# Kernel optimization log

Measured on AMD Instinct MI355X. Metric: run time of the kernel, lower is better.

## Reference

```python
import jax, jax.numpy as jnp
import numpy as np

N_NODES = 100000
N_EDGES = 1600000
D_IN, D_HID, N_CLASS = 256, 64, 40


def setup_inputs() -> dict:
    key = jax.random.key(0)
    ks = jax.random.split(key, 8)
    x = jax.random.normal(ks[0], (N_NODES, D_IN), dtype=jnp.float32)
    edge_src = jax.random.randint(ks[1], (N_EDGES,), 0, N_NODES, dtype=jnp.int64)
    edge_dst = jax.random.randint(ks[2], (N_EDGES,), 0, N_NODES, dtype=jnp.int64)
    edge_weight = jax.random.uniform(ks[3], (N_EDGES,), dtype=jnp.float32)
    W1 = jax.random.normal(ks[4], (D_IN, D_HID), dtype=jnp.float32) * (1.0 / np.sqrt(D_IN))
    b1 = jnp.zeros((D_HID,), dtype=jnp.float32)
    W2 = jax.random.normal(ks[5], (D_HID, N_CLASS), dtype=jnp.float32) * (1.0 / np.sqrt(D_HID))
    b2 = jnp.zeros((N_CLASS,), dtype=jnp.float32)
    return {"x": x, "edge_src": edge_src, "edge_dst": edge_dst,
            "edge_weight": edge_weight, "W1": W1, "b1": b1, "W2": W2, "b2": b2}


def _gcn_layer(h, W, b, edge_src, edge_dst, edge_weight):
    # support = h @ W  (dense transform), then sparse adj matmul:
    # out[dst] += w * support[src]
    support = h @ W                              # [N, d_out]
    msgs = edge_weight[:, None] * support[edge_src]  # [E, d_out] gather
    agg = jax.ops.segment_sum(msgs, edge_dst, num_segments=N_NODES)
    return agg + b


def reference(x, edge_src, edge_dst, edge_weight, W1, b1, W2, b2):
    # dropout prob = 0.0 -> identity (deterministic reference)
    h = _gcn_layer(x, W1, b1, edge_src, edge_dst, edge_weight)
    h = _gcn_layer(h, W2, b2, edge_src, edge_dst, edge_weight)
    return jax.nn.log_softmax(h, axis=1)
```

## Files before the change

kernel.cpp:

```cpp
#include <hip/hip_runtime.h>
#include <hip/hip_fp16.h>
#include <math.h>

#define N_NODES 100000
#define N_EDGES 1600000
#define D_IN    256
#define D_HID   64
#define N_CLASS 40

#define SCAN_CHUNK 256
#define SCAN_NB    ((N_NODES + SCAN_CHUNK - 1) / SCAN_CHUNK)
#define SLOT_MAX   48
#define GEMM_NB    ((N_NODES + 255) / 256)
#define FILL_NB    ((N_EDGES + 255) / 256)
#define TSTRIDE    64

__global__ __launch_bounds__(256) void prep_kernel(
    const float* __restrict__ W1, const float* __restrict__ W2,
    const float* __restrict__ b1, float* __restrict__ W12t, float* __restrict__ c1)
{
    int idx = blockIdx.x * 256 + threadIdx.x;
    if (idx < D_IN * N_CLASS) {
        int k = idx / N_CLASS;
        int c = idx - k * N_CLASS;
        float s = 0.f;
#pragma unroll
        for (int j = 0; j < D_HID; ++j)
            s = fmaf(W1[k * D_HID + j], W2[j * N_CLASS + c], s);
        W12t[c * D_IN + k] = s;
    }
    if (blockIdx.x == 0 && threadIdx.x < N_CLASS) {
        int c = threadIdx.x;
        float s = 0.f;
#pragma unroll
        for (int j = 0; j < D_HID; ++j)
            s = fmaf(b1[j], W2[j * N_CLASS + c], s);
        c1[c] = s;
    }
}

__device__ __forceinline__ void gemm_body(
    int gblk, int tid,
    const float* __restrict__ x, const float* __restrict__ W12t,
    __half* __restrict__ T, float* xs, float* wt)
{
    const int row0 = gblk * 256;

    for (int i = tid; i < N_CLASS * D_IN; i += 256) {
        int c = i >> 8;
        int k = i & 255;
        wt[c * 260 + k] = W12t[i];
    }

    const int rg = tid >> 2;
    const int cg = tid & 3;
    const int c0 = cg * 10;

    float acc[4][10];
#pragma unroll
    for (int r = 0; r < 4; ++r)
#pragma unroll
        for (int j = 0; j < 10; ++j) acc[r][j] = 0.f;

    const float4* x4 = (const float4*)x;
    float4* xs4 = (float4*)xs;
    const float4* wt4 = (const float4*)wt;

    for (int kb = 0; kb < 8; ++kb) {
        __syncthreads();
#pragma unroll
        for (int ph = 0; ph < 8; ++ph) {
            int i = ph * 256 + tid;
            int r  = i >> 3;
            int c4 = i & 7;
            int grow = min(row0 + r, N_NODES - 1);
            float4 v = x4[(size_t)grow * 64 + kb * 8 + c4];
            xs4[r * 8 + (c4 ^ ((r >> 2) & 7))] = v;
        }
        __syncthreads();

#pragma unroll
        for (int k4 = 0; k4 < 8; ++k4) {
            float4 xv[4];
#pragma unroll
            for (int r = 0; r < 4; ++r)
                xv[r] = xs4[(rg * 4 + r) * 8 + (k4 ^ (rg & 7))];
#pragma unroll
            for (int j = 0; j < 10; ++j) {
                float4 w = wt4[(c0 + j) * 65 + kb * 8 + k4];
#pragma unroll
                for (int r = 0; r < 4; ++r)
                    acc[r][j] = fmaf(xv[r].x, w.x,
                                fmaf(xv[r].y, w.y,
                                fmaf(xv[r].z, w.z,
                                fmaf(xv[r].w, w.w, acc[r][j]))));
            }
        }
    }

#pragma unroll
    for (int r = 0; r < 4; ++r) {
        int row = row0 + rg * 4 + r;
        if (row < N_NODES) {
            __half2* Trow = (__half2*)(T + (size_t)row * TSTRIDE + c0);
#pragma unroll
            for (int q = 0; q < 5; ++q)
                Trow[q] = __floats2half2_rn(acc[r][2 * q], acc[r][2 * q + 1]);
        }
    }
}

__global__ __launch_bounds__(256) void gemm_fill_kernel(
    const float* __restrict__ x, const float* __restrict__ W12t,
    __half* __restrict__ T,
    const int* __restrict__ esrc, const int* __restrict__ edst,
    const float* __restrict__ ew, int* __restrict__ cnt,
    int2* __restrict__ slots)
{
    __shared__ float xs[256 * 32];
    __shared__ float wt[N_CLASS * 260];
    const int tid = threadIdx.x;

    if (blockIdx.x < GEMM_NB) {
        gemm_body(blockIdx.x, tid, x, W12t, T, xs, wt);
    } else {
        int e = (blockIdx.x - GEMM_NB) * 256 + tid;
        if (e < N_EDGES) {
            int   d = edst[e];
            int   s = esrc[e];
            float w = ew[e];
            int slot = atomicAdd(&cnt[d], 1);
            if (slot < SLOT_MAX)
                slots[(size_t)d * SLOT_MAX + slot] =
                    make_int2(s, __float_as_int(w));
        }
    }
}

__global__ __launch_bounds__(256) void gemm_t_kernel(
    const float* __restrict__ x, const float* __restrict__ W12t,
    __half* __restrict__ T)
{
    __shared__ float xs[256 * 32];
    __shared__ float wt[N_CLASS * 260];
    gemm_body(blockIdx.x, threadIdx.x, x, W12t, T, xs, wt);
}

__global__ __launch_bounds__(256) void hist_kernel(
    const int* __restrict__ edst, int* __restrict__ cnt)
{
    int e = blockIdx.x * 256 + threadIdx.x;
    if (e >= N_EDGES) return;
    atomicAdd(&cnt[edst[e]], 1);
}

__global__ __launch_bounds__(256) void scan_partial_kernel(
    const int* __restrict__ cnt, int* __restrict__ bsum)
{
    __shared__ int red[256];
    int t = threadIdx.x;
    int idx = blockIdx.x * SCAN_CHUNK + t;
    int v = (idx < N_NODES) ? cnt[idx] : 0;
    red[t] = v;
    __syncthreads();
#pragma unroll
    for (int off = 128; off > 0; off >>= 1) {
        if (t < off) red[t] += red[t + off];
        __syncthreads();
    }
    if (t == 0) bsum[blockIdx.x] = red[0];
}

__global__ __launch_bounds__(512) void scan_block_kernel(
    const int* __restrict__ bsum, int* __restrict__ boff)
{
    __shared__ int s[512];
    int t = threadIdx.x;
    int v = (t < SCAN_NB) ? bsum[t] : 0;
    s[t] = v;
    __syncthreads();
#pragma unroll
    for (int off = 1; off < 512; off <<= 1) {
        int u = (t >= off) ? s[t - off] : 0;
        __syncthreads();
        s[t] += u;
        __syncthreads();
    }
    if (t < SCAN_NB) boff[t] = s[t] - v;
}

__global__ __launch_bounds__(256) void scan_final_kernel(
    const int* __restrict__ cnt, const int* __restrict__ boff,
    int* __restrict__ row_ptr)
{
    __shared__ int s[256];
    int t = threadIdx.x;
    int idx = blockIdx.x * SCAN_CHUNK + t;
    int v = (idx < N_NODES) ? cnt[idx] : 0;
    s[t] = v;
    __syncthreads();
#pragma unroll
    for (int off = 1; off < 256; off <<= 1) {
        int u = (t >= off) ? s[t - off] : 0;
        __syncthreads();
        s[t] += u;
        __syncthreads();
    }
    if (idx < N_NODES) row_ptr[idx] = boff[blockIdx.x] + s[t] - v;
}

__global__ __launch_bounds__(256) void fill_kernel(
    const int* __restrict__ esrc, const int* __restrict__ edst,
    const float* __restrict__ ew, int* __restrict__ row_ptr,
    int2* __restrict__ edges_s)
{
    int e = blockIdx.x * 256 + threadIdx.x;
    if (e >= N_EDGES) return;
    int d = edst[e];
    int pos = atomicAdd(&row_ptr[d], 1);
    edges_s[pos] = make_int2(esrc[e], __float_as_int(ew[e]));
}

template<bool SLOTS, bool SMAX>
__global__ __launch_bounds__(256) void agg_kernel(
    const int2* __restrict__ edges_s, const int* __restrict__ meta,
    const __half* __restrict__ Tin, void* __restrict__ Tout,
    const float* __restrict__ c1, const float* __restrict__ b2)
{
    __shared__ float red[25][11];
    __shared__ float wsh[25];
    const int t = threadIdx.x;
    const int nl  = t / 10;
    const int sub = t % 10;
    const int node = blockIdx.x * 25 + nl;
    const bool active = (t < 250) && (node < N_NODES);

    int beg = 0, end = 0;
    if (active) {
        if (SLOTS) {
            beg = node * SLOT_MAX;
            int c = meta[node];
            end = beg + (c > SLOT_MAX ? SLOT_MAX : c);
        } else {
            beg = node ? meta[node - 1] : 0;
            end = meta[node];
        }
    }

    const uint2* Tin8 = (const uint2*)Tin;
    float4 acc = make_float4(0.f, 0.f, 0.f, 0.f);
    float wsum = 0.f;

    int e = beg;
    for (; e + 7 < end; e += 8) {
        int2 a[8];
        uint2 g[8];
#pragma unroll
        for (int q = 0; q < 8; ++q) a[q] = edges_s[e + q];
#pragma unroll
        for (int q = 0; q < 8; ++q) g[q] = Tin8[a[q].x * 16 + sub];
#pragma unroll
        for (int q = 0; q < 8; ++q) {
            float w = __int_as_float(a[q].y);
            float2 f0 = __half22float2(*(const __half2*)&g[q].x);
            float2 f1 = __half22float2(*(const __half2*)&g[q].y);
            acc.x = fmaf(w, f0.x, acc.x);
            acc.y = fmaf(w, f0.y, acc.y);
            acc.z = fmaf(w, f1.x, acc.z);
            acc.w = fmaf(w, f1.y, acc.w);
            if (SMAX) wsum += w;
        }
    }
    for (; e < end; ++e) {
        int2 a0 = edges_s[e];
        float w0 = __int_as_float(a0.y);
        uint2 g0 = Tin8[a0.x * 16 + sub];
        float2 f0 = __half22float2(*(const __half2*)&g0.x);
        float2 f1 = __half22float2(*(const __half2*)&g0.y);
        acc.x = fmaf(w0, f0.x, acc.x);
        acc.y = fmaf(w0, f0.y, acc.y);
        acc.z = fmaf(w0, f1.x, acc.z);
        acc.w = fmaf(w0, f1.y, acc.w);
        if (SMAX) wsum += w0;
    }

    if (!SMAX) {
        if (active) {
            uint2 o;
            *(__half2*)&o.x = __floats2half2_rn(acc.x, acc.y);
            *(__half2*)&o.y = __floats2half2_rn(acc.z, acc.w);
            ((uint2*)Tout)[(size_t)node * 16 + sub] = o;
        }
        return;
    }

    if (active && sub == 0) wsh[nl] = wsum;
    __syncthreads();
    float dw = active ? wsh[nl] : 0.f;

    float4 cv = ((const float4*)c1)[sub];
    float4 bv = ((const float4*)b2)[sub];
    float4 z;
    z.x = fmaf(dw, cv.x, acc.x + bv.x);
    z.y = fmaf(dw, cv.y, acc.y + bv.y);
    z.z = fmaf(dw, cv.z, acc.z + bv.z);
    z.w = fmaf(dw, cv.w, acc.w + bv.w);

    float m4 = fmaxf(fmaxf(z.x, z.y), fmaxf(z.z, z.w));
    if (active) red[nl][sub] = m4;
    __syncthreads();
    float m = -INFINITY;
    if (active)
#pragma unroll
        for (int j = 0; j < 10; ++j) m = fmaxf(m, red[nl][j]);
    __syncthreads();

    float s4 = expf(z.x - m) + expf(z.y - m) + expf(z.z - m) + expf(z.w - m);
    if (active) red[nl][sub] = s4;
    __syncthreads();
    if (active) {
        float s = 0.f;
#pragma unroll
        for (int j = 0; j < 10; ++j) s += red[nl][j];
        float ls = m + logf(s);
        float4 o;
        o.x = z.x - ls; o.y = z.y - ls; o.z = z.z - ls; o.w = z.w - ls;
        ((float4*)Tout)[(size_t)node * 10 + sub] = o;
    }
}

extern "C" void kernel_launch(void* const* d_in, const int* in_sizes, int n_in,
                              void* d_out, int out_size, void* d_ws, size_t ws_size,
                              hipStream_t stream)
{
    const float* x    = (const float*)d_in[0];
    const int*   esrc = (const int*)  d_in[1];
    const int*   edst = (const int*)  d_in[2];
    const float* ew   = (const float*)d_in[3];
    const float* W1   = (const float*)d_in[4];
    const float* b1   = (const float*)d_in[5];
    const float* W2   = (const float*)d_in[6];
    const float* b2   = (const float*)d_in[7];
    float* out = (float*)d_out;

    char* ws = (char*)d_ws;
    const size_t SLOTS_BYTES = (size_t)N_NODES * SLOT_MAX * 8;
    const size_t NEED_SLOTS  = SLOTS_BYTES + 32000000 + 1000000;
    const bool use_slots = (ws_size >= NEED_SLOTS);

    if (use_slots) {
        int2*   slots = (int2*)  (ws);
        __half* T     = (__half*)(ws + SLOTS_BYTES);
        __half* Y1    = (__half*)(ws + SLOTS_BYTES + 16000000);
        int*    cnt   = (int*)   (ws + SLOTS_BYTES + 32000000);
        float*  W12t  = (float*) (ws + SLOTS_BYTES + 32400000);
        float*  c1    = (float*) (ws + SLOTS_BYTES + 32441984);

        hipMemsetAsync(cnt, 0, 400000, stream);
        prep_kernel<<<(D_IN * N_CLASS + 255) / 256, 256, 0, stream>>>(W1, W2, b1, W12t, c1);
        gemm_fill_kernel<<<GEMM_NB + FILL_NB, 256, 0, stream>>>(
            x, W12t, T, esrc, edst, ew, cnt, slots);
        agg_kernel<true, false><<<(N_NODES + 24) / 25, 256, 0, stream>>>(
            slots, cnt, T, Y1, nullptr, nullptr);
        agg_kernel<true, true><<<(N_NODES + 24) / 25, 256, 0, stream>>>(
            slots, cnt, Y1, out, c1, b2);
    } else {
        __half* T       = (__half*)(ws);
        __half* Y1      = (__half*)(ws + 16000000);
        int2*   edges_s = (int2*)  (ws + 32000000);
        int*    row_ptr = (int*)   (ws + 44800000);
        int*    cnt     = (int*)   (ws + 45200016);
        float*  W12t    = (float*) (ws + 45600016);
        float*  c1      = (float*) (ws + 45640976);
        int*    bsum    = (int*)   (ws + 45641200);
        int*    boff    = (int*)   (ws + 45642800);

        hipMemsetAsync(cnt, 0, 400000, stream);
        prep_kernel<<<(D_IN * N_CLASS + 255) / 256, 256, 0, stream>>>(W1, W2, b1, W12t, c1);
        gemm_t_kernel<<<GEMM_NB, 256, 0, stream>>>(x, W12t, T);
        hist_kernel<<<FILL_NB, 256, 0, stream>>>(edst, cnt);
        scan_partial_kernel<<<SCAN_NB, 256, 0, stream>>>(cnt, bsum);
        scan_block_kernel<<<1, 512, 0, stream>>>(bsum, boff);
        scan_final_kernel<<<SCAN_NB, 256, 0, stream>>>(cnt, boff, row_ptr);
        fill_kernel<<<FILL_NB, 256, 0, stream>>>(esrc, edst, ew, row_ptr, edges_s);
        agg_kernel<false, false><<<(N_NODES + 24) / 25, 256, 0, stream>>>(
            edges_s, row_ptr, T, Y1, nullptr, nullptr);
        agg_kernel<false, true><<<(N_NODES + 24) / 25, 256, 0, stream>>>(
            edges_s, row_ptr, Y1, out, c1, b2);
    }
}
```

Before: 342.5 us.

## Partition edge slot fill by destination range per XCD, split from GEMM

Separates the fused GEMM+edge-fill launch into two kernels. The new fill kernel assigns each block to one of 8 destination-node ranges using blockIdx&7, which presumably matches round-robin dispatch across MI355X XCDs, so atomics and slot writes for a node stay within one XCD's L2. Each group scans all edges and skips those outside its range. That makes the edge array be read 8 times, and the fill no longer overlaps with the GEMM.

```diff
diff --git a/kernel.cpp b/kernel.cpp
--- a/kernel.cpp
+++ b/kernel.cpp
@@ -12,8 +12,11 @@
 #define SCAN_NB    ((N_NODES + SCAN_CHUNK - 1) / SCAN_CHUNK)
 #define SLOT_MAX   48
 #define GEMM_NB    ((N_NODES + 255) / 256)
-#define FILL_NB    ((N_EDGES + 255) / 256)
+#define EDGE_NB    ((N_EDGES + 255) / 256)
 #define TSTRIDE    64
+#define NXCD       8
+#define XRANGE     ((N_NODES + NXCD - 1) / NXCD)
+#define FILLX_NB   2048
 
 __global__ __launch_bounds__(256) void prep_kernel(
     const float* __restrict__ W1, const float* __restrict__ W2,
@@ -110,23 +113,29 @@
     }
 }
 
-__global__ __launch_bounds__(256) void gemm_fill_kernel(
+__global__ __launch_bounds__(256) void gemm_t_kernel(
     const float* __restrict__ x, const float* __restrict__ W12t,
-    __half* __restrict__ T,
+    __half* __restrict__ T)
+{
+    __shared__ float xs[256 * 32];
+    __shared__ float wt[N_CLASS * 260];
+    gemm_body(blockIdx.x, threadIdx.x, x, W12t, T, xs, wt);
+}
+
+__global__ __launch_bounds__(256) void fill_xcd_kernel(
     const int* __restrict__ esrc, const int* __restrict__ edst,
     const float* __restrict__ ew, int* __restrict__ cnt,
     int2* __restrict__ slots)
 {
-    __shared__ float xs[256 * 32];
-    __shared__ float wt[N_CLASS * 260];
-    const int tid = threadIdx.x;
-
-    if (blockIdx.x < GEMM_NB) {
-        gemm_body(blockIdx.x, tid, x, W12t, T, xs, wt);
-    } else {
-        int e = (blockIdx.x - GEMM_NB) * 256 + tid;
-        if (e < N_EDGES) {
-            int   d = edst[e];
+    const int grp = blockIdx.x & 7;
+    const int sub = blockIdx.x >> 3;
+    const int dlo = grp * XRANGE;
+    const int dhi = min(dlo + XRANGE, N_NODES);
+    const int stride = (FILLX_NB / NXCD) * 256;
+
+    for (int e = sub * 256 + threadIdx.x; e < N_EDGES; e += stride) {
+        int d = edst[e];
+        if (d >= dlo && d < dhi) {
             int   s = esrc[e];
             float w = ew[e];
             int slot = atomicAdd(&cnt[d], 1);
@@ -135,15 +144,6 @@
                     make_int2(s, __float_as_int(w));
         }
     }
-}
-
-__global__ __launch_bounds__(256) void gemm_t_kernel(
-    const float* __restrict__ x, const float* __restrict__ W12t,
-    __half* __restrict__ T)
-{
-    __shared__ float xs[256 * 32];
-    __shared__ float wt[N_CLASS * 260];
-    gemm_body(blockIdx.x, threadIdx.x, x, W12t, T, xs, wt);
 }
 
 __global__ __launch_bounds__(256) void hist_kernel(
@@ -358,8 +358,8 @@
 
         hipMemsetAsync(cnt, 0, 400000, stream);
         prep_kernel<<<(D_IN * N_CLASS + 255) / 256, 256, 0, stream>>>(W1, W2, b1, W12t, c1);
-        gemm_fill_kernel<<<GEMM_NB + FILL_NB, 256, 0, stream>>>(
-            x, W12t, T, esrc, edst, ew, cnt, slots);
+        fill_xcd_kernel<<<FILLX_NB, 256, 0, stream>>>(esrc, edst, ew, cnt, slots);
+        gemm_t_kernel<<<GEMM_NB, 256, 0, stream>>>(x, W12t, T);
         agg_kernel<true, false><<<(N_NODES + 24) / 25, 256, 0, stream>>>(
             slots, cnt, T, Y1, nullptr, nullptr);
         agg_kernel<true, true><<<(N_NODES + 24) / 25, 256, 0, stream>>>(
@@ -378,11 +378,11 @@
         hipMemsetAsync(cnt, 0, 400000, stream);
         prep_kernel<<<(D_IN * N_CLASS + 255) / 256, 256, 0, stream>>>(W1, W2, b1, W12t, c1);
         gemm_t_kernel<<<GEMM_NB, 256, 0, stream>>>(x, W12t, T);
-        hist_kernel<<<FILL_NB, 256, 0, stream>>>(edst, cnt);
+        hist_kernel<<<EDGE_NB, 256, 0, stream>>>(edst, cnt);
         scan_partial_kernel<<<SCAN_NB, 256, 0, stream>>>(cnt, bsum);
         scan_block_kernel<<<1, 512, 0, stream>>>(bsum, boff);
         scan_final_kernel<<<SCAN_NB, 256, 0, stream>>>(cnt, boff, row_ptr);
-        fill_kernel<<<FILL_NB, 256, 0, stream>>>(esrc, edst, ew, row_ptr, edges_s);
+        fill_kernel<<<EDGE_NB, 256, 0, stream>>>(esrc, edst, ew, row_ptr, edges_s);
         agg_kernel<false, false><<<(N_NODES + 24) / 25, 256, 0, stream>>>(
             edges_s, row_ptr, T, Y1, nullptr, nullptr);
         agg_kernel<false, true><<<(N_NODES + 24) / 25, 256, 0, stream>>>(
```

Result: slower. 373.3 us (+9.0%).
